# Performance work log

Measured on AMD Instinct MI355X. Metric: run time of the kernel, lower is better.

## Reference

```python
import jax, jax.numpy as jnp
import numpy as np

B, S, D, H = 2, 2048, 1024, 16
DK = D // H

def setup_inputs() -> dict:
    key = jax.random.key(0)
    ks = jax.random.split(key, 12)
    s = 1.0 / np.sqrt(D)
    return {
        "q": jax.random.normal(ks[0], (B, S, D), jnp.float32),
        "k": jax.random.normal(ks[1], (B, S, D), jnp.float32),
        "v": jax.random.normal(ks[2], (B, S, D), jnp.float32),
        "mask": jnp.ones((1, 1, S, S), jnp.int32),
        "Wq": jax.random.normal(ks[3], (D, D), jnp.float32) * s,
        "bq": jnp.zeros((D,), jnp.float32),
        "Wk": jax.random.normal(ks[4], (D, D), jnp.float32) * s,
        "bk": jnp.zeros((D,), jnp.float32),
        "Wv": jax.random.normal(ks[5], (D, D), jnp.float32) * s,
        "bv": jnp.zeros((D,), jnp.float32),
        "Wo": jax.random.normal(ks[6], (D, D), jnp.float32) * s,
        "bo": jnp.zeros((D,), jnp.float32),
    }

def reference(q, k, v, mask, Wq, bq, Wk, bk, Wv, bv, Wo, bo):
    # projections (torch Linear: x @ W^T + b)
    Q = q @ Wq.T + bq
    K = k @ Wk.T + bk
    V = v @ Wv.T + bv
    # split heads: [B,S,D] -> [B,H,S,DK]
    def split(x):
        return x.reshape(B, S, H, DK).transpose(0, 2, 1, 3)
    Qh, Kh, Vh = split(Q), split(K), split(V)
    scores = jnp.einsum('bhqd,bhkd->bhqk', Qh, Kh) / jnp.sqrt(jnp.float32(DK))
    scores = jnp.where(mask == 0, jnp.float32(-1e9), scores)
    attn = jax.nn.softmax(scores, axis=-1)  # dropout p=0.0 -> identity
    x = jnp.einsum('bhqk,bhkd->bhqd', attn, Vh)
    x = x.transpose(0, 2, 1, 3).reshape(B, S, D)
    return x @ Wo.T + bo
```

## Files before the change

kernel.cpp:

```cpp
#include <hip/hip_runtime.h>
#include <hip/hip_bf16.h>
#include <stdint.h>

#define B_    2
#define S_    2048
#define D_    1024
#define H_    16
#define NTOK  (B_ * S_)

typedef __attribute__((ext_vector_type(8))) short bf16x8;
typedef __attribute__((ext_vector_type(4))) float f32x4;
typedef __attribute__((ext_vector_type(2))) float float2v;
typedef __attribute__((ext_vector_type(2))) __bf16 bfv2;

static __device__ __forceinline__ unsigned int pkbf(float a, float b) {
    float2v fv = {a, b};
    bfv2 r = __builtin_convertvector(fv, bfv2);
    unsigned int u;
    __builtin_memcpy(&u, &r, 4);
    return u;
}

using g_cu32 = __attribute__((address_space(1))) const unsigned int;
using l_u32  = __attribute__((address_space(3))) unsigned int;
static __device__ __forceinline__ void gld16(const void* g, void* l) {
    __builtin_amdgcn_global_load_lds((g_cu32*)g, (l_u32*)l, 16, 0, 0);
}

template<int N> static __device__ __forceinline__ void wait_vm() {
    if constexpr (N == 0)      asm volatile("s_waitcnt vmcnt(0)" ::: "memory");
    else if constexpr (N == 2) asm volatile("s_waitcnt vmcnt(2)" ::: "memory");
    else if constexpr (N == 3) asm volatile("s_waitcnt vmcnt(3)" ::: "memory");
    else if constexpr (N == 4) asm volatile("s_waitcnt vmcnt(4)" ::: "memory");
}

#define QN ((size_t)NTOK * D_)
#define WN ((size_t)D_ * D_)

struct SwapT { static constexpr bool value = true; };
struct NoSwapT { static constexpr bool value = false; };

__global__ __launch_bounds__(256) void prep_kernel(
    const float* __restrict__ q, const float* __restrict__ k, const float* __restrict__ v,
    const float* __restrict__ Wq, const float* __restrict__ Wk,
    const float* __restrict__ Wv, const float* __restrict__ Wo,
    const int* __restrict__ mask,
    unsigned short* __restrict__ qb, unsigned short* __restrict__ kb,
    unsigned short* __restrict__ vb, unsigned short* __restrict__ wqb,
    unsigned short* __restrict__ wkb, unsigned short* __restrict__ wvb,
    unsigned short* __restrict__ wob, int* __restrict__ flags) {
    __shared__ int anyz;
    if (blockIdx.x < 8192) {
        size_t i = ((size_t)blockIdx.x * 256 + threadIdx.x) * 8;
        const float* s; unsigned short* d; size_t off;
        if (i < QN)          { s = q; d = qb; off = i; }
        else if (i < 2 * QN) { s = k; d = kb; off = i - QN; }
        else if (i < 3 * QN) { s = v; d = vb; off = i - 2 * QN; }
        else {
            size_t j = i - 3 * QN;
            int wi = (int)(j >> 20);
            s = (wi == 0) ? Wq : (wi == 1) ? Wk : (wi == 2) ? Wv : Wo;
            d = (wi == 0) ? wqb : (wi == 1) ? wkb : (wi == 2) ? wvb : wob;
            off = j & (WN - 1);
        }
        float4 a = *(const float4*)(s + off);
        float4 b = *(const float4*)(s + off + 4);
        uint4 pk;
        pk.x = pkbf(a.x, a.y); pk.y = pkbf(a.z, a.w);
        pk.z = pkbf(b.x, b.y); pk.w = pkbf(b.z, b.w);
        *(uint4*)(d + off) = pk;
    } else {
        if (threadIdx.x == 0) anyz = 0;
        __syncthreads();
        int bid2 = blockIdx.x - 8192;
        const int qt = bid2 >> 5, kt = bid2 & 31;
        int az = 0;
        for (int i = threadIdx.x; i < 64 * 64; i += 256) {
            int r = i >> 6, c = i & 63;
            az |= (mask[(size_t)(qt * 64 + r) * S_ + kt * 64 + c] == 0) ? 1 : 0;
        }
        if (az) atomicOr(&anyz, 1);
        __syncthreads();
        if (threadIdx.x == 0) flags[qt * 32 + kt] = anyz;
    }
}

struct GemmArgs {
    const unsigned short* A[3];
    const unsigned short* W[3];
    const float* bias[3];
    void* C[3];
    int mode[3];
    float scale[3];
};

template<int BMT>
__global__ __launch_bounds__(256, 3) void gemm_async(GemmArgs ga) {
    constexpr int AG = BMT / 16;
    constexpr int MI = BMT / 32;
    constexpr int NK = D_ / 32;
    constexpr int LOADS = (BMT == 128) ? 4 : 3;
    constexpr int MT = NTOK / BMT;
    constexpr int PERZ = MT * 8;

    const int bid = blockIdx.x;
    const int nb8 = (int)gridDim.x >> 3;
    const int l = (bid & 7) * nb8 + (bid >> 3);
    const int z = l / PERZ;
    const int r = l % PERZ;
    const int bx = r % MT;
    const int by = r / MT;

    const unsigned short* __restrict__ A = ga.A[z];
    const unsigned short* __restrict__ W = ga.W[z];
    const float* __restrict__ bias = ga.bias[z];
    void* C = ga.C[z];
    const int mode = ga.mode[z];
    const float scl = ga.scale[z];

    __shared__ unsigned short As[3][AG * 512];
    __shared__ unsigned short Bs[3][8 * 512];

    const int t    = threadIdx.x;
    const int lane = t & 63;
    const int w    = t >> 6;
    const int fr   = lane & 15;
    const int kq   = lane >> 4;
    const int wrow = w >> 1, wcol = w & 1;
    const int m0 = bx * BMT, n0 = by * 128;

    const int sc = lane >> 4;
    const int sr = lane & 15;

    const unsigned short* ga0;
    const unsigned short* ga1 = nullptr;
    int la0Off, la1Off = 0;
    if constexpr (BMT == 128) {
        ga0 = A + (size_t)(m0 + (2 * w) * 16 + sr) * D_ + sc * 8;
        ga1 = ga0 + 16 * D_;
        la0Off = (2 * w) * 512;
        la1Off = (2 * w + 1) * 512;
    } else {
        ga0 = A + (size_t)(m0 + w * 16 + sr) * D_ + sc * 8;
        la0Off = w * 512;
    }
    const unsigned short* gw0 = W + (size_t)(n0 + (2 * w) * 16 + sr) * D_ + sc * 8;
    const unsigned short* gw1 = gw0 + 16 * D_;
    const int lw0Off = (2 * w) * 512;
    const int lw1Off = (2 * w + 1) * 512;

    int aOff[MI], bOff[4];
#pragma unroll
    for (int mi = 0; mi < MI; ++mi) aOff[mi] = (wrow * MI + mi) * 512 + (kq * 16 + fr) * 8;
#pragma unroll
    for (int ni = 0; ni < 4; ++ni) bOff[ni] = (wcol * 4 + ni) * 512 + (kq * 16 + fr) * 8;

    f32x4 acc[MI][4];
#pragma unroll
    for (int i = 0; i < MI; ++i)
#pragma unroll
        for (int j = 0; j < 4; ++j) acc[i][j] = (f32x4)0.0f;

    auto stage = [&](int buf) {
        gld16(ga0, &As[buf][la0Off]);
        if constexpr (BMT == 128) gld16(ga1, &As[buf][la1Off]);
        gld16(gw0, &Bs[buf][lw0Off]);
        gld16(gw1, &Bs[buf][lw1Off]);
        ga0 += 32; gw0 += 32; gw1 += 32;
        if constexpr (BMT == 128) ga1 += 32;
    };

    auto kloop = [&](auto swc) {
        constexpr bool SW = decltype(swc)::value;
        auto mma_step = [&](int cur) {
            const unsigned short* Ab = As[cur];
            const unsigned short* Bb = Bs[cur];
            bf16x8 af[MI], bfr[4];
#pragma unroll
            for (int mi = 0; mi < MI; ++mi) af[mi] = *(const bf16x8*)&Ab[aOff[mi]];
#pragma unroll
            for (int ni = 0; ni < 4; ++ni) bfr[ni] = *(const bf16x8*)&Bb[bOff[ni]];
#pragma unroll
            for (int mi = 0; mi < MI; ++mi)
#pragma unroll
                for (int ni = 0; ni < 4; ++ni) {
                    if constexpr (SW)
                        acc[mi][ni] = __builtin_amdgcn_mfma_f32_16x16x32_bf16(
                            bfr[ni], af[mi], acc[mi][ni], 0, 0, 0);
                    else
                        acc[mi][ni] = __builtin_amdgcn_mfma_f32_16x16x32_bf16(
                            af[mi], bfr[ni], acc[mi][ni], 0, 0, 0);
                }
        };

        stage(0);
        stage(1);
        int cur = 0;
        for (int k0 = 0; k0 < NK - 1; ++k0) {
            __builtin_amdgcn_sched_barrier(0);
            wait_vm<LOADS>();
            __builtin_amdgcn_s_barrier();
            __builtin_amdgcn_sched_barrier(0);
            if (k0 + 2 < NK) {
                int pf = (cur >= 1) ? cur - 1 : cur + 2;
                stage(pf);
            }
            mma_step(cur);
            cur = (cur < 2) ? cur + 1 : 0;
        }
        __builtin_amdgcn_sched_barrier(0);
        wait_vm<0>();
        __builtin_amdgcn_s_barrier();
        __builtin_amdgcn_sched_barrier(0);
        mma_step(cur);
    };
    if (mode == 2) kloop(NoSwapT{}); else kloop(SwapT{});

    if (mode == 2) {
        unsigned short* Co = (unsigned short*)C;
#pragma unroll
        for (int ni = 0; ni < 4; ++ni) {
            int col = n0 + wcol * 64 + ni * 16 + fr;
            float bv = bias[col];
            int hh = col >> 6, d = col & 63;
#pragma unroll
            for (int mi = 0; mi < MI; ++mi) {
                int tok = m0 + wrow * (BMT / 2) + mi * 16 + kq * 4;
                int bb = tok >> 11, sbase = tok & (S_ - 1);
                uint2 pk;
                pk.x = pkbf((acc[mi][ni][0] + bv) * scl, (acc[mi][ni][1] + bv) * scl);
                pk.y = pkbf((acc[mi][ni][2] + bv) * scl, (acc[mi][ni][3] + bv) * scl);
                *(uint2*)(Co + ((size_t)((bb * H_ + hh) * 64 + d)) * S_ + sbase) = pk;
            }
        }
    } else if (mode == 0) {
        float* Co = (float*)C;
#pragma unroll
        for (int ni = 0; ni < 4; ++ni) {
            int nb = n0 + wcol * 64 + ni * 16 + kq * 4;
            float4 b4 = *(const float4*)&bias[nb];
#pragma unroll
            for (int mi = 0; mi < MI; ++mi) {
                int m = m0 + wrow * (BMT / 2) + mi * 16 + fr;
                float4 o4;
                o4.x = (acc[mi][ni][0] + b4.x) * scl;
                o4.y = (acc[mi][ni][1] + b4.y) * scl;
                o4.z = (acc[mi][ni][2] + b4.z) * scl;
                o4.w = (acc[mi][ni][3] + b4.w) * scl;
                *(float4*)(Co + (size_t)m * D_ + nb) = o4;
            }
        }
    } else {
        unsigned short* Co = (unsigned short*)C;
#pragma unroll
        for (int ni = 0; ni < 4; ++ni) {
            int nb = n0 + wcol * 64 + ni * 16 + kq * 4;
            float4 b4 = *(const float4*)&bias[nb];
#pragma unroll
            for (int mi = 0; mi < MI; ++mi) {
                int m = m0 + wrow * (BMT / 2) + mi * 16 + fr;
                uint2 pk;
                pk.x = pkbf((acc[mi][ni][0] + b4.x) * scl, (acc[mi][ni][1] + b4.y) * scl);
                pk.y = pkbf((acc[mi][ni][2] + b4.z) * scl, (acc[mi][ni][3] + b4.w) * scl);
                *(uint2*)(Co + (size_t)m * D_ + nb) = pk;
            }
        }
    }
}

__global__ __launch_bounds__(512, 2) void flash4(
    const unsigned short* __restrict__ Qb, const unsigned short* __restrict__ Kb,
    const unsigned short* __restrict__ Vtg, const int* __restrict__ mask,
    const int* __restrict__ flags, unsigned short* __restrict__ Xb) {
    __shared__ unsigned short Ks[3][4096];
    __shared__ unsigned short Vs[3][4096];
    __shared__ unsigned short Ps[16384];

    const int t    = threadIdx.x;
    const int lane = t & 63;
    const int w    = t >> 6;
    const int fr   = lane & 15;
    const int kq   = lane >> 4;
    const int bid = blockIdx.x;
    const int swb = ((bid & 7) << 5) | (bid >> 3);
    const int qt = swb & 7, hd = (swb >> 3) & 15, b = swb >> 7;
    const int q0 = qt * 256;
    const int swz = fr & 7;

    bf16x8 qf[2][2];
#pragma unroll
    for (int qc = 0; qc < 2; ++qc) {
        const unsigned short* qrow_p =
            Qb + (size_t)(b * S_ + q0 + w * 32 + qc * 16 + fr) * D_ + hd * 64;
        qf[qc][0] = *(const bf16x8*)(qrow_p + kq * 8);
        qf[qc][1] = *(const bf16x8*)(qrow_p + 32 + kq * 8);
    }

    unsigned int fmask[2];
#pragma unroll
    for (int qc = 0; qc < 2; ++qc) {
        int qt64 = qt * 4 + ((2 * w + qc) >> 2);
        int fl = (lane < 32) ? flags[qt64 * 32 + lane] : 0;
        fmask[qc] = (unsigned int)__ballot(fl != 0);
    }

    const unsigned short* kptr =
        Kb + (size_t)(b * S_ + (w >> 1) * 16 + fr) * D_ + hd * 64 + (w & 1) * 32 + kq * 8;
    const unsigned short* vptr =
        Vtg + ((size_t)((b * H_ + hd) * 64 + (w >> 1) * 16 + fr)) * S_ + (w & 1) * 32 + kq * 8;

    gld16(kptr, (char*)&Ks[0][0] + w * 1024);
    gld16(vptr, (char*)&Vs[0][0] + w * 1024);
    gld16(kptr + (size_t)64 * D_, (char*)&Ks[1][0] + w * 1024);
    gld16(vptr + 64,              (char*)&Vs[1][0] + w * 1024);
    const unsigned short* kpf = kptr + (size_t)128 * D_;
    const unsigned short* vpf = vptr + 128;

    unsigned short* pswr[2][4];
    const unsigned short* psrd[2][2];
#pragma unroll
    for (int qc = 0; qc < 2; ++qc) {
        int row = w * 32 + qc * 16 + fr;
#pragma unroll
        for (int mi = 0; mi < 4; ++mi) {
            int chunk = mi * 2 + (kq >> 1);
            pswr[qc][mi] = &Ps[row * 64 + ((chunk ^ swz) << 3) + ((kq & 1) << 2)];
        }
#pragma unroll
        for (int kk = 0; kk < 2; ++kk) {
            int c = kk * 4 + kq;
            psrd[qc][kk] = &Ps[row * 64 + ((c ^ swz) << 3)];
        }
    }

    const f32x4 zf = (f32x4)0.0f;
    f32x4 o[2][4];
#pragma unroll
    for (int qc = 0; qc < 2; ++qc)
#pragma unroll
        for (int i = 0; i < 4; ++i) o[qc][i] = zf;
    float2v l2[2];
    l2[0] = (float2v){0.0f, 0.0f};
    l2[1] = (float2v){0.0f, 0.0f};

    auto attn_step = [&](int cur, int kt) {
        f32x4 st[2][4];
#pragma unroll
        for (int mi = 0; mi < 4; ++mi) {
            bf16x8 a = *(const bf16x8*)&Ks[cur][mi * 1024 + (kq * 16 + fr) * 8];
            st[0][mi] = __builtin_amdgcn_mfma_f32_16x16x32_bf16(a, qf[0][0], zf, 0, 0, 0);
            st[1][mi] = __builtin_amdgcn_mfma_f32_16x16x32_bf16(a, qf[1][0], zf, 0, 0, 0);
        }
#pragma unroll
        for (int mi = 0; mi < 4; ++mi) {
            bf16x8 a = *(const bf16x8*)&Ks[cur][mi * 1024 + ((4 + kq) * 16 + fr) * 8];
            st[0][mi] = __builtin_amdgcn_mfma_f32_16x16x32_bf16(a, qf[0][1], st[0][mi], 0, 0, 0);
            st[1][mi] = __builtin_amdgcn_mfma_f32_16x16x32_bf16(a, qf[1][1], st[1][mi], 0, 0, 0);
        }

#pragma unroll
        for (int qc = 0; qc < 2; ++qc) {
            if ((fmask[qc] >> kt) & 1u) {
#pragma unroll
                for (int mi = 0; mi < 4; ++mi) {
                    int4 mv = *(const int4*)&mask[(size_t)(q0 + w * 32 + qc * 16 + fr) * S_ +
                                                  kt * 64 + mi * 16 + kq * 4];
                    if (mv.x == 0) st[qc][mi][0] = -3e8f;
                    if (mv.y == 0) st[qc][mi][1] = -3e8f;
                    if (mv.z == 0) st[qc][mi][2] = -3e8f;
                    if (mv.w == 0) st[qc][mi][3] = -3e8f;
                }
            }
        }

#pragma unroll
        for (int qc = 0; qc < 2; ++qc)
#pragma unroll
            for (int mi = 0; mi < 4; ++mi) {
                float e0 = __builtin_amdgcn_exp2f(st[qc][mi][0]);
                float e1 = __builtin_amdgcn_exp2f(st[qc][mi][1]);
                float e2 = __builtin_amdgcn_exp2f(st[qc][mi][2]);
                float e3 = __builtin_amdgcn_exp2f(st[qc][mi][3]);
                l2[qc] += (float2v){e0, e1} + (float2v){e2, e3};
                uint2 pk;
                pk.x = pkbf(e0, e1);
                pk.y = pkbf(e2, e3);
                *(uint2*)pswr[qc][mi] = pk;
            }

#pragma unroll
        for (int kk = 0; kk < 2; ++kk) {
            bf16x8 pb0 = *(const bf16x8*)psrd[0][kk];
            bf16x8 pb1 = *(const bf16x8*)psrd[1][kk];
#pragma unroll
            for (int mi = 0; mi < 4; ++mi) {
                bf16x8 a = *(const bf16x8*)&Vs[cur][mi * 1024 + ((kk * 4 + kq) * 16 + fr) * 8];
                o[0][mi] = __builtin_amdgcn_mfma_f32_16x16x32_bf16(a, pb0, o[0][mi], 0, 0, 0);
                o[1][mi] = __builtin_amdgcn_mfma_f32_16x16x32_bf16(a, pb1, o[1][mi], 0, 0, 0);
            }
        }
    };

    int cur = 0;
    for (int kt = 0; kt < 31; ++kt) {
        __builtin_amdgcn_sched_barrier(0);
        wait_vm<2>();
        __builtin_amdgcn_s_barrier();
        __builtin_amdgcn_sched_barrier(0);
        if (kt < 30) {
            int pf = (cur >= 1) ? cur - 1 : cur + 2;
            gld16(kpf, (char*)&Ks[pf][0] + w * 1024);
            gld16(vpf, (char*)&Vs[pf][0] + w * 1024);
            kpf += (size_t)64 * D_;
            vpf += 64;
        }
        attn_step(cur, kt);
        cur = (cur < 2) ? cur + 1 : 0;
    }
    __builtin_amdgcn_sched_barrier(0);
    wait_vm<0>();
    __builtin_amdgcn_s_barrier();
    __builtin_amdgcn_sched_barrier(0);
    attn_step(cur, 31);

#pragma unroll
    for (int qc = 0; qc < 2; ++qc) {
        float l_i = l2[qc].x + l2[qc].y;
        l_i += __shfl_xor(l_i, 16, 64);
        l_i += __shfl_xor(l_i, 32, 64);
        float rl = 1.0f / l_i;
#pragma unroll
        for (int mi = 0; mi < 4; ++mi) {
            uint2 pk;
            pk.x = pkbf(o[qc][mi][0] * rl, o[qc][mi][1] * rl);
            pk.y = pkbf(o[qc][mi][2] * rl, o[qc][mi][3] * rl);
            *(uint2*)(Xb + (size_t)(b * S_ + q0 + w * 32 + qc * 16 + fr) * D_ +
                      hd * 64 + mi * 16 + kq * 4) = pk;
        }
    }
}

extern "C" void kernel_launch(void* const* d_in, const int* in_sizes, int n_in,
                              void* d_out, int out_size, void* d_ws, size_t ws_size,
                              hipStream_t stream) {
    const float* q    = (const float*)d_in[0];
    const float* k    = (const float*)d_in[1];
    const float* v    = (const float*)d_in[2];
    const int*   mask = (const int*)d_in[3];
    const float* Wq   = (const float*)d_in[4];
    const float* bq   = (const float*)d_in[5];
    const float* Wk   = (const float*)d_in[6];
    const float* bk   = (const float*)d_in[7];
    const float* Wv   = (const float*)d_in[8];
    const float* bv   = (const float*)d_in[9];
    const float* Wo   = (const float*)d_in[10];
    const float* bo   = (const float*)d_in[11];
    float* out = (float*)d_out;

    unsigned short* qb  = (unsigned short*)d_ws;
    unsigned short* kb  = qb + QN;
    unsigned short* vb  = kb + QN;
    unsigned short* Qf  = vb + QN;
    unsigned short* Kf  = Qf + QN;
    unsigned short* Vt  = Kf + QN;
    unsigned short* wqb = Vt + QN;
    unsigned short* wkb = wqb + WN;
    unsigned short* wvb = wkb + WN;
    unsigned short* wob = wvb + WN;
    int* flags = (int*)(wob + WN);

    const float SC = 0.18033688011112042f;

    prep_kernel<<<9216, 256, 0, stream>>>(q, k, v, Wq, Wk, Wv, Wo, mask,
                                          qb, kb, vb, wqb, wkb, wvb, wob, flags);

    GemmArgs g1;
    g1.A[0] = qb;  g1.W[0] = wqb; g1.bias[0] = bq; g1.C[0] = Qf; g1.mode[0] = 1; g1.scale[0] = SC;
    g1.A[1] = kb;  g1.W[1] = wkb; g1.bias[1] = bk; g1.C[1] = Kf; g1.mode[1] = 1; g1.scale[1] = 1.0f;
    g1.A[2] = vb;  g1.W[2] = wvb; g1.bias[2] = bv; g1.C[2] = Vt; g1.mode[2] = 2; g1.scale[2] = 1.0f;
    gemm_async<128><<<768, 256, 0, stream>>>(g1);

    flash4<<<256, 512, 0, stream>>>(Qf, Kf, Vt, mask, flags, Qf);

    GemmArgs g2;
    g2.A[0] = Qf; g2.W[0] = wob; g2.bias[0] = bo; g2.C[0] = out; g2.mode[0] = 0; g2.scale[0] = 1.0f;
    g2.A[1] = g2.A[2] = nullptr; g2.W[1] = g2.W[2] = nullptr;
    g2.bias[1] = g2.bias[2] = nullptr; g2.C[1] = g2.C[2] = nullptr;
    g2.mode[1] = g2.mode[2] = 0; g2.scale[1] = g2.scale[2] = 1.0f;
    gemm_async<64><<<512, 256, 0, stream>>>(g2);
}
```

Before: 266.7 us.

## Replace QKV projection GEMM with 128x64-tile, 2-wave double-buffered kernel

Adds a new gemm_n64 kernel for the fused Q/K/V projections. It uses 128x64 output tiles, 128 threads per block and a unified double-buffered LDS with 12 load groups, and it waits on lgkmcnt plus a barrier before issuing the next prefetch. The launch doubles the grid to 1536 blocks to improve wave balance across CUs. gemm_async is trimmed to serve only the fp32 output projection, with its mode branches removed. The new kernel keeps 2 stages instead of 3 and adds an extra barrier per k-step, which may expose more load latency.

Measured after the change: 285.4 us. 1.07x slower.

```diff
diff --git a/kernel.cpp b/kernel.cpp
--- a/kernel.cpp
+++ b/kernel.cpp
@@ -32,6 +32,10 @@
     else if constexpr (N == 2) asm volatile("s_waitcnt vmcnt(2)" ::: "memory");
     else if constexpr (N == 3) asm volatile("s_waitcnt vmcnt(3)" ::: "memory");
     else if constexpr (N == 4) asm volatile("s_waitcnt vmcnt(4)" ::: "memory");
+    else if constexpr (N == 6) asm volatile("s_waitcnt vmcnt(6)" ::: "memory");
+}
+static __device__ __forceinline__ void wait_lgkm0() {
+    asm volatile("s_waitcnt lgkmcnt(0)" ::: "memory");
 }
 
 #define QN ((size_t)NTOK * D_)
@@ -94,6 +98,140 @@
     float scale[3];
 };
 
+__global__ __launch_bounds__(128, 3) void gemm_n64(GemmArgs ga) {
+    constexpr int NK = D_ / 32;
+    constexpr int AG = 8;
+    constexpr int NG = 12;
+    constexpr int GPW = 6;
+    const int bid = blockIdx.x;
+    const int l = (bid & 7) * 192 + (bid >> 3);
+    const int z = l >> 9;
+    const int r = l & 511;
+    const int bx = r & 31;
+    const int by = r >> 5;
+
+    const unsigned short* __restrict__ A = ga.A[z];
+    const unsigned short* __restrict__ W = ga.W[z];
+    const float* __restrict__ bias = ga.bias[z];
+    void* C = ga.C[z];
+    const int mode = ga.mode[z];
+    const float scl = ga.scale[z];
+
+    __shared__ unsigned short Ls[2][NG * 512];
+
+    const int t    = threadIdx.x;
+    const int lane = t & 63;
+    const int w    = t >> 6;
+    const int fr   = lane & 15;
+    const int kq   = lane >> 4;
+    const int m0 = bx * 128, n0 = by * 64;
+
+    const int sc = lane >> 4;
+    const int sr = lane & 15;
+
+    const unsigned short* gp[GPW];
+    int ldo[GPW];
+#pragma unroll
+    for (int j = 0; j < GPW; ++j) {
+        int g = w * GPW + j;
+        if (g < AG) gp[j] = A + (size_t)(m0 + g * 16 + sr) * D_ + sc * 8;
+        else        gp[j] = W + (size_t)(n0 + (g - AG) * 16 + sr) * D_ + sc * 8;
+        ldo[j] = g * 512;
+    }
+
+    int aOff[4], bOff[4];
+#pragma unroll
+    for (int mi = 0; mi < 4; ++mi) aOff[mi] = (w * 4 + mi) * 512 + (kq * 16 + fr) * 8;
+#pragma unroll
+    for (int ni = 0; ni < 4; ++ni) bOff[ni] = (AG + ni) * 512 + (kq * 16 + fr) * 8;
+
+    f32x4 acc[4][4];
+#pragma unroll
+    for (int i = 0; i < 4; ++i)
+#pragma unroll
+        for (int j = 0; j < 4; ++j) acc[i][j] = (f32x4)0.0f;
+
+    auto stage = [&](int buf) {
+#pragma unroll
+        for (int j = 0; j < GPW; ++j) {
+            gld16(gp[j], &Ls[buf][ldo[j]]);
+            gp[j] += 32;
+        }
+    };
+
+    auto kloop = [&](auto swc) {
+        constexpr bool SW = decltype(swc)::value;
+        stage(0);
+        stage(1);
+        for (int k0 = 0; k0 < NK; ++k0) {
+            const int cur = k0 & 1;
+            __builtin_amdgcn_sched_barrier(0);
+            if (k0 < NK - 1) wait_vm<GPW>();
+            else             wait_vm<0>();
+            __builtin_amdgcn_s_barrier();
+            __builtin_amdgcn_sched_barrier(0);
+
+            bf16x8 af[4], bfr[4];
+#pragma unroll
+            for (int mi = 0; mi < 4; ++mi) af[mi] = *(const bf16x8*)&Ls[cur][aOff[mi]];
+#pragma unroll
+            for (int ni = 0; ni < 4; ++ni) bfr[ni] = *(const bf16x8*)&Ls[cur][bOff[ni]];
+
+            wait_lgkm0();
+            __builtin_amdgcn_sched_barrier(0);
+            __builtin_amdgcn_s_barrier();
+            if (k0 + 2 < NK) stage(cur);
+
+#pragma unroll
+            for (int mi = 0; mi < 4; ++mi)
+#pragma unroll
+                for (int ni = 0; ni < 4; ++ni) {
+                    if constexpr (SW)
+                        acc[mi][ni] = __builtin_amdgcn_mfma_f32_16x16x32_bf16(
+                            bfr[ni], af[mi], acc[mi][ni], 0, 0, 0);
+                    else
+                        acc[mi][ni] = __builtin_amdgcn_mfma_f32_16x16x32_bf16(
+                            af[mi], bfr[ni], acc[mi][ni], 0, 0, 0);
+                }
+        }
+    };
+    if (mode == 2) kloop(NoSwapT{}); else kloop(SwapT{});
+
+    if (mode == 2) {
+        unsigned short* Co = (unsigned short*)C;
+#pragma unroll
+        for (int ni = 0; ni < 4; ++ni) {
+            int col = n0 + ni * 16 + fr;
+            float bv = bias[col];
+            int hh = col >> 6, d = col & 63;
+#pragma unroll
+            for (int mi = 0; mi < 4; ++mi) {
+                int tok = m0 + w * 64 + mi * 16 + kq * 4;
+                int bb = tok >> 11, sbase = tok & (S_ - 1);
+                uint2 pk;
+                pk.x = pkbf((acc[mi][ni][0] + bv) * scl, (acc[mi][ni][1] + bv) * scl);
+                pk.y = pkbf((acc[mi][ni][2] + bv) * scl, (acc[mi][ni][3] + bv) * scl);
+                *(uint2*)(Co + ((size_t)((bb * H_ + hh) * 64 + d)) * S_ + sbase) = pk;
+            }
+        }
+    } else {
+        unsigned short* Co = (unsigned short*)C;
+#pragma unroll
+        for (int ni = 0; ni < 4; ++ni) {
+            int nb = n0 + ni * 16 + kq * 4;
+            float4 b4 = *(const float4*)&bias[nb];
+#pragma unroll
+            for (int mi = 0; mi < 4; ++mi) {
+                int m = m0 + w * 64 + mi * 16 + fr;
+                uint2 pk;
+                pk.x = pkbf((acc[mi][ni][0] + b4.x) * scl, (acc[mi][ni][1] + b4.y) * scl);
+                pk.y = pkbf((acc[mi][ni][2] + b4.z) * scl, (acc[mi][ni][3] + b4.w) * scl);
+                *(uint2*)(Co + (size_t)m * D_ + nb) = pk;
+            }
+        }
+    }
+}
+
 template<int BMT>
 __global__ __launch_bounds__(256, 3) void gemm_async(GemmArgs ga) {
     constexpr int AG = BMT / 16;
@@ -115,7 +253,6 @@
     const unsigned short* __restrict__ W = ga.W[z];
     const float* __restrict__ bias = ga.bias[z];
     void* C = ga.C[z];
-    const int mode = ga.mode[z];
     const float scl = ga.scale[z];
 
     __shared__ unsigned short As[3][AG * 512];
@@ -132,18 +269,8 @@
     const int sc = lane >> 4;
     const int sr = lane & 15;
 
-    const unsigned short* ga0;
-    const unsigned short* ga1 = nullptr;
-    int la0Off, la1Off = 0;
-    if constexpr (BMT == 128) {
-        ga0 = A + (size_t)(m0 + (2 * w) * 16 + sr) * D_ + sc * 8;
-        ga1 = ga0 + 16 * D_;
-        la0Off = (2 * w) * 512;
-        la1Off = (2 * w + 1) * 512;
-    } else {
-        ga0 = A + (size_t)(m0 + w * 16 + sr) * D_ + sc * 8;
-        la0Off = w * 512;
-    }
+    const unsigned short* ga0 = A + (size_t)(m0 + w * 16 + sr) * D_ + sc * 8;
+    const int la0Off = w * 512;
     const unsigned short* gw0 = W + (size_t)(n0 + (2 * w) * 16 + sr) * D_ + sc * 8;
     const unsigned short* gw1 = gw0 + 16 * D_;
     const int lw0Off = (2 * w) * 512;
@@ -163,107 +290,62 @@
 
     auto stage = [&](int buf) {
         gld16(ga0, &As[buf][la0Off]);
-        if constexpr (BMT == 128) gld16(ga1, &As[buf][la1Off]);
         gld16(gw0, &Bs[buf][lw0Off]);
         gld16(gw1, &Bs[buf][lw1Off]);
         ga0 += 32; gw0 += 32; gw1 += 32;
-        if constexpr (BMT == 128) ga1 += 32;
     };
 
-    auto kloop = [&](auto swc) {
-        constexpr bool SW = decltype(swc)::value;
-        auto mma_step = [&](int cur) {
-            const unsigned short* Ab = As[cur];
-            const unsigned short* Bb = Bs[cur];
-            bf16x8 af[MI], bfr[4];
-#pragma unroll
-            for (int mi = 0; mi < MI; ++mi) af[mi] = *(const bf16x8*)&Ab[aOff[mi]];
-#pragma unroll
-            for (int ni = 0; ni < 4; ++ni) bfr[ni] = *(const bf16x8*)&Bb[bOff[ni]];
-#pragma unroll
-            for (int mi = 0; mi < MI; ++mi)
-#pragma unroll
-                for (int ni = 0; ni < 4; ++ni) {
-                    if constexpr (SW)
-                        acc[mi][ni] = __builtin_amdgcn_mfma_f32_16x16x32_bf16(
-                            bfr[ni], af[mi], acc[mi][ni], 0, 0, 0);
-                    else
-                        acc[mi][ni] = __builtin_amdgcn_mfma_f32_16x16x32_bf16(
-                            af[mi], bfr[ni], acc[mi][ni], 0, 0, 0);
-                }
-        };
-
-        stage(0);
-        stage(1);
-        int cur = 0;
-        for (int k0 = 0; k0 < NK - 1; ++k0) {
-            __builtin_amdgcn_sched_barrier(0);
-            wait_vm<LOADS>();
-            __builtin_amdgcn_s_barrier();
-            __builtin_amdgcn_sched_barrier(0);
-            if (k0 + 2 < NK) {
-                int pf = (cur >= 1) ? cur - 1 : cur + 2;
-                stage(pf);
-            }
-            mma_step(cur);
-            cur = (cur < 2) ? cur + 1 : 0;
-        }
+    auto mma_step = [&](int cur) {
+        const unsigned short* Ab = As[cur];
+        const unsigned short* Bb = Bs[cur];
+        bf16x8 af[MI], bfr[4];
+#pragma unroll
+        for (int mi = 0; mi < MI; ++mi) af[mi] = *(const bf16x8*)&Ab[aOff[mi]];
+#pragma unroll
+        for (int ni = 0; ni < 4; ++ni) bfr[ni] = *(const bf16x8*)&Bb[bOff[ni]];
+#pragma unroll
+        for (int mi = 0; mi < MI; ++mi)
+#pragma unroll
+            for (int ni = 0; ni < 4; ++ni)
+                acc[mi][ni] = __builtin_amdgcn_mfma_f32_16x16x32_bf16(
+                    bfr[ni], af[mi], acc[mi][ni], 0, 0, 0);
+    };
+
+    stage(0);
+    stage(1);
+    int cur = 0;
+    for (int k0 = 0; k0 < NK - 1; ++k0) {
         __builtin_amdgcn_sched_barrier(0);
-        wait_vm<0>();
+        wait_vm<LOADS>();
         __builtin_amdgcn_s_barrier();
         __builtin_amdgcn_sched_barrier(0);
+        if (k0 + 2 < NK) {
+            int pf = (cur >= 1) ? cur - 1 : cur + 2;
+            stage(pf);
+        }
         mma_step(cur);
-    };
-    if (mode == 2) kloop(NoSwapT{}); else kloop(SwapT{});
-
-    if (mode == 2) {
-        unsigned short* Co = (unsigned short*)C;
-#pragma unroll
-        for (int ni = 0; ni < 4; ++ni) {
-            int col = n0 + wcol * 64 + ni * 16 + fr;
-            float bv = bias[col];
-            int hh = col >> 6, d = col & 63;
-#pragma unroll
-            for (int mi = 0; mi < MI; ++mi) {
-                int tok = m0 + wrow * (BMT / 2) + mi * 16 + kq * 4;
-                int bb = tok >> 11, sbase = tok & (S_ - 1);
-                uint2 pk;
-                pk.x = pkbf((acc[mi][ni][0] + bv) * scl, (acc[mi][ni][1] + bv) * scl);
-                pk.y = pkbf((acc[mi][ni][2] + bv) * scl, (acc[mi][ni][3] + bv) * scl);
-                *(uint2*)(Co + ((size_t)((bb * H_ + hh) * 64 + d)) * S_ + sbase) = pk;
-            }
-        }
-    } else if (mode == 0) {
-        float* Co = (float*)C;
-#pragma unroll
-        for (int ni = 0; ni < 4; ++ni) {
-            int nb = n0 + wcol * 64 + ni * 16 + kq * 4;
-            float4 b4 = *(const float4*)&bias[nb];
-#pragma unroll
-            for (int mi = 0; mi < MI; ++mi) {
-                int m = m0 + wrow * (BMT / 2) + mi * 16 + fr;
-                float4 o4;
-                o4.x = (acc[mi][ni][0] + b4.x) * scl;
-                o4.y = (acc[mi][ni][1] + b4.y) * scl;
-                o4.z = (acc[mi][ni][2] + b4.z) * scl;
-                o4.w = (acc[mi][ni][3] + b4.w) * scl;
-                *(float4*)(Co + (size_t)m * D_ + nb) = o4;
-            }
-        }
-    } else {
-        unsigned short* Co = (unsigned short*)C;
-#pragma unroll
-        for (int ni = 0; ni < 4; ++ni) {
-            int nb = n0 + wcol * 64 + ni * 16 + kq * 4;
-            float4 b4 = *(const float4*)&bias[nb];
-#pragma unroll
-            for (int mi = 0; mi < MI; ++mi) {
-                int m = m0 + wrow * (BMT / 2) + mi * 16 + fr;
-                uint2 pk;
-                pk.x = pkbf((acc[mi][ni][0] + b4.x) * scl, (acc[mi][ni][1] + b4.y) * scl);
-                pk.y = pkbf((acc[mi][ni][2] + b4.z) * scl, (acc[mi][ni][3] + b4.w) * scl);
-                *(uint2*)(Co + (size_t)m * D_ + nb) = pk;
-            }
+        cur = (cur < 2) ? cur + 1 : 0;
+    }
+    __builtin_amdgcn_sched_barrier(0);
+    wait_vm<0>();
+    __builtin_amdgcn_s_barrier();
+    __builtin_amdgcn_sched_barrier(0);
+    mma_step(cur);
+
+    float* Co = (float*)C;
+#pragma unroll
+    for (int ni = 0; ni < 4; ++ni) {
+        int nb = n0 + wcol * 64 + ni * 16 + kq * 4;
+        float4 b4 = *(const float4*)&bias[nb];
+#pragma unroll
+        for (int mi = 0; mi < MI; ++mi) {
+            int m = m0 + wrow * (BMT / 2) + mi * 16 + fr;
+            float4 o4;
+            o4.x = (acc[mi][ni][0] + b4.x) * scl;
+            o4.y = (acc[mi][ni][1] + b4.y) * scl;
+            o4.z = (acc[mi][ni][2] + b4.z) * scl;
+            o4.w = (acc[mi][ni][3] + b4.w) * scl;
+            *(float4*)(Co + (size_t)m * D_ + nb) = o4;
         }
     }
 }
@@ -478,7 +560,7 @@
     g1.A[0] = qb;  g1.W[0] = wqb; g1.bias[0] = bq; g1.C[0] = Qf; g1.mode[0] = 1; g1.scale[0] = SC;
     g1.A[1] = kb;  g1.W[1] = wkb; g1.bias[1] = bk; g1.C[1] = Kf; g1.mode[1] = 1; g1.scale[1] = 1.0f;
     g1.A[2] = vb;  g1.W[2] = wvb; g1.bias[2] = bv; g1.C[2] = Vt; g1.mode[2] = 2; g1.scale[2] = 1.0f;
-    gemm_async<128><<<768, 256, 0, stream>>>(g1);
+    gemm_n64<<<1536, 128, 0, stream>>>(g1);
 
     flash4<<<256, 512, 0, stream>>>(Qf, Kf, Vt, mask, flags, Qf);
 
```
